# Kernel tuning notes

Measured on AMD Instinct MI355X. Metric: run time of the kernel, lower is better.

Reference implementation:

```python
import jax, jax.numpy as jnp
import numpy as np

NUM_TOKENS = 1048576
TOP_K = 8
N_EXPERTS = 64
BLOCK = 128


def setup_inputs() -> dict:
    key = jax.random.key(0)
    topk_ids = jax.random.randint(key, (NUM_TOKENS, TOP_K), 0, N_EXPERTS, dtype=jnp.int32)
    return {"topk_ids": topk_ids, "num_experts": N_EXPERTS, "block_size": BLOCK}


def reference(topk_ids, num_experts, block_size):
    # Faithful re-implementation of sgl_kernel.moe_align_block_size with
    # E_eff = num_experts + 1 experts and pad_sorted_token_ids=True.
    flat = topk_ids.reshape(-1).astype(jnp.int32)
    T = flat.shape[0]                              # total routed tokens
    E = num_experts + 1                            # kernel is called with E+1
    M = T + E * (block_size - 1)                   # max_num_tokens_padded
    num_blocks = M // block_size                   # max_num_m_blocks

    # per-expert histogram and block-aligned (padded) counts
    counts = jnp.bincount(flat, length=E).astype(jnp.int32)
    padded = ((counts + block_size - 1) // block_size) * block_size

    cum_pad = jnp.cumsum(padded).astype(jnp.int32)          # inclusive padded cumsum
    off_pad = jnp.concatenate([jnp.zeros(1, jnp.int32), cum_pad[:-1]])  # exclusive
    cum_cnt = jnp.cumsum(counts).astype(jnp.int32)
    off_cnt = jnp.concatenate([jnp.zeros(1, jnp.int32), cum_cnt[:-1]])

    # stable sort token indices by expert id; rank within expert = sorted pos - start
    order = jnp.argsort(flat, stable=True).astype(jnp.int32)
    sorted_e = flat[order]
    j = jnp.arange(T, dtype=jnp.int32)
    pos = off_pad[sorted_e] + (j - off_cnt[sorted_e])

    # padding slots hold T (= topk_ids.numel()), matching pad_sorted_token_ids=True
    sorted_token_ids = jnp.full((M,), T, dtype=jnp.int32).at[pos].set(order)

    # expert id per M-block; blocks beyond the padded total stay 0 (torch.zeros init)
    bstart = jnp.arange(num_blocks, dtype=jnp.int32) * block_size
    eid = jnp.searchsorted(cum_pad, bstart, side='right').astype(jnp.int32)
    total = cum_pad[-1]
    expert_ids = jnp.where(bstart < total, eid, 0).astype(jnp.int32)

    num_tokens_post_pad = total.reshape(1).astype(jnp.int32)
    return sorted_token_ids, expert_ids, num_tokens_post_pad
```

## Files before the change

### kernel.cpp

```cpp
#include <hip/hip_runtime.h>
#include <stdint.h>

#define NE 64
#define E  65
#define BLK 128
#define CHB 64

#define T1 512
#define W1 8
#define TPB1 8192
#define NB1 1024
#define NC1 16

#define THREADS 256
#define WPB 4
#define TPB 4096


__global__ void __launch_bounds__(T1) k_rank(const int* __restrict__ topk,
                                             uint32_t* __restrict__ packed,
                                             int* __restrict__ wcnt,
                                             int* __restrict__ bcnt) {
    __shared__ int lrun[W1][NE];
    const int tid = threadIdx.x, w = tid >> 6, lane = tid & 63;
    const int b = blockIdx.x;
    lrun[w][lane] = 0;
    const int wstart = b * TPB1 + w * 1024;
    uint32_t pk[8];
#pragma unroll
    for (int it = 0; it < 16; ++it) {
        int e = topk[wstart + it * 64 + lane] & 63;
        int r = atomicAdd(&lrun[w][e], 1);
        uint32_t p = ((uint32_t)e << 10) | (uint32_t)r;
        if (it & 1) pk[it >> 1] |= p; else pk[it >> 1] = p << 16;
    }
#pragma unroll
    for (int q = 0; q < 8; ++q)
        packed[(size_t)b * 4096 + w * 512 + q * 64 + lane] = pk[q];
    wcnt[b * (W1 * NE) + w * NE + lane] = lrun[w][lane];
    __syncthreads();
    if (tid < NE) {
        int s = 0;
#pragma unroll
        for (int w2 = 0; w2 < W1; ++w2) s += lrun[w2][tid];
        bcnt[b * NE + tid] = s;
    }
}

__global__ void k_scan1(int* __restrict__ bcnt, int* __restrict__ ctot) {
    __shared__ int tile[CHB * NE];
    const int c = blockIdx.x, tid = threadIdx.x;
    for (int i = tid; i < CHB * NE; i += THREADS) tile[i] = bcnt[c * CHB * NE + i];
    __syncthreads();
    if (tid < NE) {
        int acc = 0;
#pragma unroll 8
        for (int j = 0; j < CHB; ++j) { int o = tile[j * NE + tid]; tile[j * NE + tid] = acc; acc += o; }
        ctot[c * NE + tid] = acc;
    }
    __syncthreads();
    for (int i = tid; i < CHB * NE; i += THREADS) bcnt[c * CHB * NE + i] = tile[i];
}

__global__ void __launch_bounds__(T1) k_sort2(
        const uint32_t* __restrict__ packed, const int* __restrict__ wcnt,
        const int* __restrict__ bpre,
        const int* __restrict__ ctot,
        int* __restrict__ sorted, int* __restrict__ eids, int* __restrict__ npp,
        int nb, int M, int T, int epb) {
    __shared__ int sbuf[TPB1];
    __shared__ int cps[E];
    const int tid = threadIdx.x, w = tid >> 6, lane = tid & 63;
    const int b = blockIdx.x, c = b >> 6;

    int ct_pre = 0, cnts = 0;
#pragma unroll
    for (int k = 0; k < NC1; ++k) {
        int v = ctot[k * NE + lane];
        ct_pre += (k < c) ? v : 0;
        cnts += v;
    }
    int padded = (cnts + BLK - 1) & ~(BLK - 1);
    int incl2 = padded;
#pragma unroll
    for (int d = 1; d < 64; d <<= 1) { int t = __shfl_up(incl2, d); if (lane >= d) incl2 += t; }
    int off_lane = incl2 - padded;
    int total = __shfl(incl2, 63);
    if (tid < NE) cps[tid] = incl2;
    if (tid == 0) cps[NE] = total;

    uint32_t pk[8];
#pragma unroll
    for (int q = 0; q < 8; ++q)
        pk[q] = packed[(size_t)b * 4096 + w * 512 + q * 64 + lane];

    int btot = 0, woff = 0;
#pragma unroll
    for (int w2 = 0; w2 < W1; ++w2) {
        int v = wcnt[b * (W1 * NE) + w2 * NE + lane];
        btot += v; woff += (w2 < w) ? v : 0;
    }
    int incl = btot;
#pragma unroll
    for (int d = 1; d < 64; d <<= 1) { int t = __shfl_up(incl, d); if (lane >= d) incl += t; }
    int loc = incl - btot;
    int S = loc + woff;
    int dbase = off_lane + ct_pre + bpre[b * NE + lane] - loc;

    const int wloc = w * 1024;
#pragma unroll
    for (int q = 0; q < 8; ++q) {
        uint32_t pw = pk[q];
        int e0 = (int)(pw >> 26) & 63, r0 = (int)((pw >> 16) & 1023);
        int e1 = (int)((pw >> 10) & 63), r1 = (int)(pw & 1023);
        int p0 = (__shfl(S, e0) + r0) & (TPB1 - 1);
        int p1 = (__shfl(S, e1) + r1) & (TPB1 - 1);
        sbuf[p0] = (e0 << 13) | (wloc + (2 * q) * 64 + lane);
        sbuf[p1] = (e1 << 13) | (wloc + (2 * q + 1) * 64 + lane);
    }
    __syncthreads();

    const int bstart = b * TPB1;
#pragma unroll
    for (int k = 0; k < TPB1 / T1; ++k) {
        int j = k * T1 + tid;
        int p = sbuf[j];
        int e = (p >> 13) & 63;
        int d = __shfl(dbase, e);
        sorted[d + j] = bstart + (p & (TPB1 - 1));
    }

    if (tid < epb) {
        int jb = b * epb + tid;
        if (jb < nb) {
            int bs2 = jb * BLK, r = 0;
            if (bs2 < total) {
                int lo = 0, hi = E;
                while (lo < hi) { int mid = (lo + hi) >> 1; if (cps[mid] <= bs2) lo = mid + 1; else hi = mid; }
                r = lo;
            }
            eids[jb] = r;
        }
    }
    if (b < NE) {
        int cc = __shfl(cnts, b);
        int ob = __shfl(off_lane, b);
        int pe = (cc + BLK - 1) & ~(BLK - 1);
        int len = pe - cc;
        if (tid < len) sorted[ob + cc + tid] = T;
    } else if (b >= E && b < E + 17) {
        int i = total + (b - E) * T1 + tid;
        if (i < M) sorted[i] = T;
    }
    if (b == 0 && tid == 0) *npp = total;
}

__global__ void __launch_bounds__(THREADS, 8) k_hist(const int* __restrict__ topk,
                                                     int* __restrict__ bcnt) {
    __shared__ int hist[WPB][NE];
    const int tid = threadIdx.x, w = tid >> 6, lane = tid & 63;
    hist[w][lane] = 0;
    const int base = blockIdx.x * TPB + w * 1024;
#pragma unroll
    for (int it = 0; it < 4; ++it) {
        int4 v = *(const int4*)(topk + base + it * 256 + lane * 4);
        atomicAdd(&hist[w][v.x & 63], 1);
        atomicAdd(&hist[w][v.y & 63], 1);
        atomicAdd(&hist[w][v.z & 63], 1);
        atomicAdd(&hist[w][v.w & 63], 1);
    }
    __syncthreads();
    if (tid < NE)
        bcnt[blockIdx.x * NE + tid] =
            hist[0][tid] + hist[1][tid] + hist[2][tid] + hist[3][tid];
}

__global__ void k_scan2(int* __restrict__ ctot, int* __restrict__ counts,
                        int* __restrict__ off_pad, int* __restrict__ cum_pad,
                        int* __restrict__ npp, int nc) {
    __shared__ int ct[32 * NE];
    const int tid = threadIdx.x;
    for (int i = tid; i < nc * NE; i += THREADS) ct[i] = ctot[i];
    __syncthreads();
    if (tid < NE) {
        int acc = 0;
        for (int c = 0; c < nc; ++c) { int o = ct[c * NE + tid]; ct[c * NE + tid] = acc; acc += o; }
        counts[tid] = acc;
    }
    if (tid == NE) counts[NE] = 0;
    __syncthreads();
    for (int i = tid; i < nc * NE; i += THREADS) ctot[i] = ct[i];
    if (tid == 0) {
        int run = 0;
        for (int e = 0; e < E; ++e) {
            int p = (counts[e] + BLK - 1) & ~(BLK - 1);
            off_pad[e] = run; run += p; cum_pad[e] = run;
        }
        *npp = run;
    }
}

__global__ void __launch_bounds__(THREADS) k_sort(
        const int* __restrict__ topk, const int* __restrict__ bpre,
        const int* __restrict__ ctot, const int* __restrict__ counts,
        const int* __restrict__ off_pad, const int* __restrict__ cum_pad,
        int* __restrict__ sorted, int* __restrict__ eids,
        int nb, int M, int T, int epb) {
    __shared__ int lrun[WPB][NE];
    __shared__ int wt[WPB][NE];
    __shared__ int sbuf[TPB];
    __shared__ int cps[E];
    const int tid = threadIdx.x, w = tid >> 6, lane = tid & 63;
    const int b = blockIdx.x, c = b / CHB;
    if (tid < E) cps[tid] = cum_pad[tid];
    lrun[w][lane] = 0;
    const int wstart = b * TPB + w * 1024;
    int packed[16];
#pragma unroll
    for (int it = 0; it < 16; ++it) {
        int e = topk[wstart + it * 64 + lane] & 63;
        int r = atomicAdd(&lrun[w][e], 1);
        packed[it] = (e << 10) | r;
    }
    wt[w][lane] = lrun[w][lane];
    __syncthreads();
    int woff = 0, btot = 0;
#pragma unroll
    for (int w2 = 0; w2 < WPB; ++w2) { int v = wt[w2][lane]; woff += (w2 < w) ? v : 0; btot += v; }
    int incl = btot;
#pragma unroll
    for (int d = 1; d < 64; d <<= 1) { int t = __shfl_up(incl, d); if (lane >= d) incl += t; }
    int loc = incl - btot;
    int dbase = off_pad[lane] + ctot[c * NE + lane] + bpre[b * NE + lane] - loc;
    int S = loc + woff;
    const int wloc = w * 1024;
#pragma unroll
    for (int it = 0; it < 16; ++it) {
        int e = packed[it] >> 10;
        int r = packed[it] & 1023;
        int pos = (__shfl(S, e) + r) & (TPB - 1);
        sbuf[pos] = (e << 12) | (wloc + it * 64 + lane);
    }
    __syncthreads();
    const int bstart = b * TPB;
#pragma unroll
    for (int k = 0; k < 16; ++k) {
        int j = k * THREADS + tid;
        int p = sbuf[j];
        int e = (p >> 12) & 63;
        int d = __shfl(dbase, e);
        sorted[d + j] = bstart + (p & 0xfff);
    }
    int total = cps[NE - 1];
    if (tid < epb) {
        int j = b * epb + tid;
        if (j < nb) {
            int bs2 = j * BLK, r = 0;
            if (bs2 < total) {
                int lo = 0, hi = E;
                while (lo < hi) { int mid = (lo + hi) >> 1; if (cps[mid] <= bs2) lo = mid + 1; else hi = mid; }
                r = lo;
            }
            eids[j] = r;
        }
    }
    if (b < E) {
        int cc = counts[b];
        int pe = (cc + BLK - 1) & ~(BLK - 1);
        int len = pe - cc;
        if (tid < len) sorted[off_pad[b] + cc + tid] = T;
    } else if (b < E + 33) {
        int i = total + (b - E) * THREADS + tid;
        if (i < M) sorted[i] = T;
    }
}

extern "C" void kernel_launch(void* const* d_in, const int* in_sizes, int n_in,
                              void* d_out, int out_size, void* d_ws, size_t ws_size,
                              hipStream_t stream) {
    const int* topk = (const int*)d_in[0];
    const int T = in_sizes[0];
    const int M = T + E * (BLK - 1);
    const int nb = M / BLK;

    int* out = (int*)d_out;
    int* sorted = out;
    int* expert_ids = out + M;
    int* npp = out + M + nb;

    bool fast = (T == NB1 * TPB1);
    size_t need = ((size_t)(T / 2) + (size_t)NB1 * W1 * NE + (size_t)NB1 * NE
                   + (size_t)NC1 * NE) * sizeof(int);
    if (need > ws_size) fast = false;

    if (fast) {
        uint32_t* packed = (uint32_t*)d_ws;
        int* wcnt = (int*)(packed + (size_t)T / 2);
        int* bcnt = wcnt + (size_t)NB1 * W1 * NE;
        int* ctot = bcnt + (size_t)NB1 * NE;
        const int epb = (nb + NB1 - 1) / NB1;

        k_rank<<<NB1, T1, 0, stream>>>(topk, packed, wcnt, bcnt);
        k_scan1<<<NC1, THREADS, 0, stream>>>(bcnt, ctot);
        k_sort2<<<NB1, T1, 0, stream>>>(packed, wcnt, bcnt, ctot,
                                        sorted, expert_ids, npp, nb, M, T, epb);
        return;
    }

    const int NB = T / TPB;
    const int NC = NB / CHB;
    const int epb = (nb + NB - 1) / NB;
    int* bcnt    = (int*)d_ws;
    int* ctot    = bcnt + (size_t)NB * NE;
    int* counts  = ctot + (size_t)NC * NE;
    int* off_pad = counts + E;
    int* cum_pad = off_pad + E;

    k_hist<<<NB, THREADS, 0, stream>>>(topk, bcnt);
    k_scan1<<<NC, THREADS, 0, stream>>>(bcnt, ctot);
    k_scan2<<<1, THREADS, 0, stream>>>(ctot, counts, off_pad, cum_pad, npp, NC);
    k_sort<<<NB, THREADS, 0, stream>>>(topk, bcnt, ctot, counts, off_pad, cum_pad,
                                       sorted, expert_ids, nb, M, T, epb);
}
```

Before: 31.20 us.

## Drop scan kernel; each sort block recomputes prefix from 16-bit block counts

```diff
diff --git a/kernel.cpp b/kernel.cpp
--- a/kernel.cpp
+++ b/kernel.cpp
@@ -10,7 +10,7 @@
 #define W1 8
 #define TPB1 8192
 #define NB1 1024
-#define NC1 16
+#define RPW (NB1 / W1)
 
 #define THREADS 256
 #define WPB 4
@@ -20,7 +20,7 @@
 __global__ void __launch_bounds__(T1) k_rank(const int* __restrict__ topk,
                                              uint32_t* __restrict__ packed,
                                              int* __restrict__ wcnt,
-                                             int* __restrict__ bcnt) {
+                                             unsigned short* __restrict__ bcnt16) {
     __shared__ int lrun[W1][NE];
     const int tid = threadIdx.x, w = tid >> 6, lane = tid & 63;
     const int b = blockIdx.x;
@@ -43,43 +43,45 @@
         int s = 0;
 #pragma unroll
         for (int w2 = 0; w2 < W1; ++w2) s += lrun[w2][tid];
-        bcnt[b * NE + tid] = s;
-    }
-}
-
-__global__ void k_scan1(int* __restrict__ bcnt, int* __restrict__ ctot) {
-    __shared__ int tile[CHB * NE];
-    const int c = blockIdx.x, tid = threadIdx.x;
-    for (int i = tid; i < CHB * NE; i += THREADS) tile[i] = bcnt[c * CHB * NE + i];
-    __syncthreads();
-    if (tid < NE) {
-        int acc = 0;
-#pragma unroll 8
-        for (int j = 0; j < CHB; ++j) { int o = tile[j * NE + tid]; tile[j * NE + tid] = acc; acc += o; }
-        ctot[c * NE + tid] = acc;
-    }
-    __syncthreads();
-    for (int i = tid; i < CHB * NE; i += THREADS) bcnt[c * CHB * NE + i] = tile[i];
+        bcnt16[b * NE + tid] = (unsigned short)s;
+    }
 }
 
 __global__ void __launch_bounds__(T1) k_sort2(
         const uint32_t* __restrict__ packed, const int* __restrict__ wcnt,
-        const int* __restrict__ bpre,
-        const int* __restrict__ ctot,
+        const unsigned short* __restrict__ bcnt16,
         int* __restrict__ sorted, int* __restrict__ eids, int* __restrict__ npp,
         int nb, int M, int T, int epb) {
     __shared__ int sbuf[TPB1];
     __shared__ int cps[E];
+    __shared__ int part_pre[W1][NE];
+    __shared__ int part_all[W1][NE];
     const int tid = threadIdx.x, w = tid >> 6, lane = tid & 63;
-    const int b = blockIdx.x, c = b >> 6;
-
+    const int b = blockIdx.x;
+
+    uint32_t pk[8];
+#pragma unroll
+    for (int q = 0; q < 8; ++q)
+        pk[q] = packed[(size_t)b * 4096 + w * 512 + q * 64 + lane];
+
+    {
+        int pre = 0, all = 0;
+        const int r0 = w * RPW;
+#pragma unroll 8
+        for (int r = 0; r < RPW; ++r) {
+            int row = r0 + r;
+            int v = (int)bcnt16[row * NE + lane];
+            all += v;
+            pre += (row < b) ? v : 0;
+        }
+        part_pre[w][lane] = pre;
+        part_all[w][lane] = all;
+    }
+    __syncthreads();
     int ct_pre = 0, cnts = 0;
 #pragma unroll
-    for (int k = 0; k < NC1; ++k) {
-        int v = ctot[k * NE + lane];
-        ct_pre += (k < c) ? v : 0;
-        cnts += v;
-    }
+    for (int w2 = 0; w2 < W1; ++w2) { ct_pre += part_pre[w2][lane]; cnts += part_all[w2][lane]; }
+
     int padded = (cnts + BLK - 1) & ~(BLK - 1);
     int incl2 = padded;
 #pragma unroll
@@ -89,11 +91,6 @@
     if (tid < NE) cps[tid] = incl2;
     if (tid == 0) cps[NE] = total;
 
-    uint32_t pk[8];
-#pragma unroll
-    for (int q = 0; q < 8; ++q)
-        pk[q] = packed[(size_t)b * 4096 + w * 512 + q * 64 + lane];
-
     int btot = 0, woff = 0;
 #pragma unroll
     for (int w2 = 0; w2 < W1; ++w2) {
@@ -105,7 +102,7 @@
     for (int d = 1; d < 64; d <<= 1) { int t = __shfl_up(incl, d); if (lane >= d) incl += t; }
     int loc = incl - btot;
     int S = loc + woff;
-    int dbase = off_lane + ct_pre + bpre[b * NE + lane] - loc;
+    int dbase = off_lane + ct_pre - loc;
 
     const int wloc = w * 1024;
 #pragma unroll
@@ -173,6 +170,21 @@
     if (tid < NE)
         bcnt[blockIdx.x * NE + tid] =
             hist[0][tid] + hist[1][tid] + hist[2][tid] + hist[3][tid];
+}
+
+__global__ void k_scan1(int* __restrict__ bcnt, int* __restrict__ ctot) {
+    __shared__ int tile[CHB * NE];
+    const int c = blockIdx.x, tid = threadIdx.x;
+    for (int i = tid; i < CHB * NE; i += THREADS) tile[i] = bcnt[c * CHB * NE + i];
+    __syncthreads();
+    if (tid < NE) {
+        int acc = 0;
+#pragma unroll 8
+        for (int j = 0; j < CHB; ++j) { int o = tile[j * NE + tid]; tile[j * NE + tid] = acc; acc += o; }
+        ctot[c * NE + tid] = acc;
+    }
+    __syncthreads();
+    for (int i = tid; i < CHB * NE; i += THREADS) bcnt[c * CHB * NE + i] = tile[i];
 }
 
 __global__ void k_scan2(int* __restrict__ ctot, int* __restrict__ counts,
@@ -289,20 +301,18 @@
     int* npp = out + M + nb;
 
     bool fast = (T == NB1 * TPB1);
-    size_t need = ((size_t)(T / 2) + (size_t)NB1 * W1 * NE + (size_t)NB1 * NE
-                   + (size_t)NC1 * NE) * sizeof(int);
+    size_t need = ((size_t)(T / 2) + (size_t)NB1 * W1 * NE) * sizeof(int)
+                + (size_t)NB1 * NE * sizeof(unsigned short);
     if (need > ws_size) fast = false;
 
     if (fast) {
         uint32_t* packed = (uint32_t*)d_ws;
         int* wcnt = (int*)(packed + (size_t)T / 2);
-        int* bcnt = wcnt + (size_t)NB1 * W1 * NE;
-        int* ctot = bcnt + (size_t)NB1 * NE;
+        unsigned short* bcnt16 = (unsigned short*)(wcnt + (size_t)NB1 * W1 * NE);
         const int epb = (nb + NB1 - 1) / NB1;
 
-        k_rank<<<NB1, T1, 0, stream>>>(topk, packed, wcnt, bcnt);
-        k_scan1<<<NC1, THREADS, 0, stream>>>(bcnt, ctot);
-        k_sort2<<<NB1, T1, 0, stream>>>(packed, wcnt, bcnt, ctot,
+        k_rank<<<NB1, T1, 0, stream>>>(topk, packed, wcnt, bcnt16);
+        k_sort2<<<NB1, T1, 0, stream>>>(packed, wcnt, bcnt16,
                                         sorted, expert_ids, npp, nb, M, T, epb);
         return;
     }
```

Result: slower. 39.65 us (+27.1%).
